# Optimization experiments

Hardware: AMD Instinct MI355X
Metric: run time of the kernel (lower is better)

## Reference

```python
import jax, jax.numpy as jnp
import numpy as np

N_EMBED = 1024
N_HEAD = 16
HEAD_DIM = N_EMBED // N_HEAD


def setup_inputs() -> dict:
    key = jax.random.key(0)
    ks = jax.random.split(key, 6)
    B, T, C = 4, 2048, N_EMBED
    scale = 1.0 / np.sqrt(C)
    x = jax.random.normal(ks[0], (B, T, C), dtype=jnp.float32)
    # torch nn.Linear weights are [out, in]; y = x @ W.T
    Wk = jax.random.normal(ks[1], (C, C), dtype=jnp.float32) * scale
    Wq = jax.random.normal(ks[2], (C, C), dtype=jnp.float32) * scale
    Wv = jax.random.normal(ks[3], (C, C), dtype=jnp.float32) * scale
    Wp = jax.random.normal(ks[4], (C, C), dtype=jnp.float32) * scale
    bp = jax.random.normal(ks[5], (C,), dtype=jnp.float32) * 0.01
    return {"x": x, "Wk": Wk, "Wq": Wq, "Wv": Wv, "Wp": Wp, "bp": bp}


def reference(x, Wk, Wq, Wv, Wp, bp):
    B, T, C = x.shape
    H, D = N_HEAD, HEAD_DIM
    # QKV projections (torch Linear: x @ W.T), split heads -> [B, H, T, D]
    k = (x @ Wk.T).reshape(B, T, H, D).transpose(0, 2, 1, 3)
    q = (x @ Wq.T).reshape(B, T, H, D).transpose(0, 2, 1, 3)
    v = (x @ Wv.T).reshape(B, T, H, D).transpose(0, 2, 1, 3)
    # scaled scores [B, H, T, T]
    att = jnp.einsum('bhtd,bhsd->bhts', q, k) * (1.0 / np.sqrt(D))
    causal = jnp.tril(jnp.ones((T, T), dtype=bool))
    att = jnp.where(causal[None, None, :, :], att, -jnp.inf)
    att = jax.nn.softmax(att, axis=-1)
    out = jnp.einsum('bhts,bhsd->bhtd', att, v)  # [B, H, T, D]
    out = out.transpose(0, 2, 1, 3).reshape(B, T, C)
    out = out @ Wp.T + bp
    return out
```

## Files before the change

### kernel.cpp

```cpp
#include <hip/hip_runtime.h>

typedef __bf16 bf16_t;
typedef bf16_t bf16x4 __attribute__((ext_vector_type(4)));
typedef bf16_t bf16x8 __attribute__((ext_vector_type(8)));
typedef float f32x4 __attribute__((ext_vector_type(4)));

#define B_ 4
#define T_ 2048
#define C_ 1024
#define H_ 16
#define D_ 64

#define GLDS(g, l)                                                          \
  __builtin_amdgcn_global_load_lds(                                         \
      (const __attribute__((address_space(1))) void*)(g),                   \
      (__attribute__((address_space(3))) void*)(l), 16, 0, 0)

static __device__ __forceinline__ f32x4 mfma16(bf16x8 a, bf16x8 b, f32x4 c) {
  return __builtin_amdgcn_mfma_f32_16x16x32_bf16(a, b, c, 0, 0, 0);
}

static __device__ __forceinline__ float exp2_hw(float x) {
  float r;
  asm("v_exp_f32 %0, %1" : "=v"(r) : "v"(x));
  return r;
}

__global__ void cvt_all(const float* __restrict__ x, const float* __restrict__ wq,
                        const float* __restrict__ wk, const float* __restrict__ wv,
                        const float* __restrict__ wp, bf16_t* __restrict__ xb,
                        bf16_t* __restrict__ wqb, bf16_t* __restrict__ wkb,
                        bf16_t* __restrict__ wvb, bf16_t* __restrict__ wpb) {
  int i = blockIdx.x * blockDim.x + threadIdx.x;
  const float* src;
  bf16_t* dst;
  int off;
  if (i < 2097152) {
    src = x; dst = xb; off = i;
  } else {
    int r = i - 2097152;
    int region = r >> 18;
    off = r & 262143;
    if (region == 0) { src = wq; dst = wqb; }
    else if (region == 1) { src = wk; dst = wkb; }
    else if (region == 2) { src = wv; dst = wvb; }
    else { src = wp; dst = wpb; }
  }
  float4 v = ((const float4*)src)[off];
  bf16x4 o = {(bf16_t)v.x, (bf16_t)v.y, (bf16_t)v.z, (bf16_t)v.w};
  ((bf16x4*)dst)[off] = o;
}

__global__ __launch_bounds__(512, 4) void gemm_qkv(
    const bf16_t* __restrict__ xb, const bf16_t* __restrict__ wq,
    const bf16_t* __restrict__ wk, const bf16_t* __restrict__ wv,
    bf16_t* __restrict__ qo, bf16_t* __restrict__ ko, bf16_t* __restrict__ vt) {
  __shared__ bf16_t lA[2][128 * 64];
  __shared__ bf16_t lB[2][3][64 * 64];
  const int tid = threadIdx.x, wave = tid >> 6, lane = tid & 63;
  const int g = lane >> 4;
  const int bid = blockIdx.x;
  const int swz = ((bid & 7) << 7) | (bid >> 3);
  const int col0 = (swz & 15) * 64, row0 = (swz >> 4) * 128;
  const int wr = wave >> 2, wc = wave & 3;
  f32x4 acc[3][4] = {};

  const int soffA[2] = {wave * 1024, (8 + wave) * 1024};
  size_t sgoA[2];
#pragma unroll
  for (int i = 0; i < 2; ++i) {
    const int lin = soffA[i] + lane * 16;
    const int r = lin >> 7;
    const int c = ((lin >> 4) & 7) ^ (r & 7);
    sgoA[i] = (size_t)r * C_ + c * 8;
  }
  const int soffB = wave * 1024;
  size_t sgoB;
  {
    const int lin = soffB + lane * 16;
    const int r = lin >> 7;
    const int c = ((lin >> 4) & 7) ^ (r & 7);
    sgoB = (size_t)r * C_ + c * 8;
  }
  int koffA[2][4], koffB[2];
#pragma unroll
  for (int s = 0; s < 2; ++s) {
    const int c = s * 4 + g;
#pragma unroll
    for (int m = 0; m < 4; ++m) {
      const int r = wr * 64 + m * 16 + (lane & 15);
      koffA[s][m] = r * 128 + ((c ^ (r & 7)) << 4);
    }
    const int rb = wc * 16 + (lane & 15);
    koffB[s] = rb * 128 + ((c ^ (rb & 7)) << 4);
  }

#define QKV_STAGE(k0, b)                                                    \
  {                                                                         \
    GLDS(xb + (size_t)row0 * C_ + (k0) + sgoA[0], &lA[b][soffA[0] >> 1]);   \
    GLDS(xb + (size_t)row0 * C_ + (k0) + sgoA[1], &lA[b][soffA[1] >> 1]);   \
    GLDS(wq + (size_t)col0 * C_ + (k0) + sgoB, &lB[b][0][soffB >> 1]);      \
    GLDS(wk + (size_t)col0 * C_ + (k0) + sgoB, &lB[b][1][soffB >> 1]);      \
    GLDS(wv + (size_t)col0 * C_ + (k0) + sgoB, &lB[b][2][soffB >> 1]);      \
  }

  QKV_STAGE(0, 0);
  int cur = 0;
  for (int k0 = 0; k0 < C_; k0 += 64) {
    __syncthreads();
    if (k0 + 64 < C_) QKV_STAGE(k0 + 64, cur ^ 1);
#pragma unroll
    for (int s = 0; s < 2; ++s) {
      const char* ab = (const char*)lA[cur];
      bf16x8 af[4];
#pragma unroll
      for (int m = 0; m < 4; ++m) af[m] = *(const bf16x8*)(ab + koffA[s][m]);
#pragma unroll
      for (int z = 0; z < 3; ++z) {
        bf16x8 bf = *(const bf16x8*)((const char*)lB[cur][z] + koffB[s]);
#pragma unroll
        for (int m = 0; m < 4; ++m) acc[z][m] = mfma16(af[m], bf, acc[z][m]);
      }
    }
    cur ^= 1;
  }
#pragma unroll
  for (int z = 0; z < 3; ++z) {
    bf16_t* outb = (z == 0) ? qo : ((z == 1) ? ko : vt);
    const float qs = (z == 0) ? 0.125f * 1.4426950408889634f : 1.0f;
    const int gc = col0 + wc * 16 + (lane & 15);
    const int h = gc >> 6, d = gc & 63;
#pragma unroll
    for (int m = 0; m < 4; ++m) {
      const int gr = row0 + wr * 64 + m * 16 + ((lane >> 4) << 2);
      const int b = gr >> 11, t = gr & (T_ - 1);
      if (z < 2) {
#pragma unroll
        for (int j = 0; j < 4; ++j)
          outb[(((size_t)(b * H_ + h)) * T_ + (t + j)) * D_ + d] =
              (bf16_t)(acc[z][m][j] * qs);
      } else {
        bf16x4 pk = {(bf16_t)acc[z][m][0], (bf16_t)acc[z][m][1],
                     (bf16_t)acc[z][m][2], (bf16_t)acc[z][m][3]};
        *(bf16x4*)(outb + (((size_t)(b * H_ + h)) * D_ + d) * T_ + t) = pk;
      }
    }
  }
}

__global__ __launch_bounds__(256) void gemm_proj(const bf16_t* __restrict__ att,
                                                 const bf16_t* __restrict__ wp,
                                                 const float* __restrict__ bias,
                                                 float* __restrict__ out) {
  __shared__ bf16_t lA[2][128 * 64];
  __shared__ bf16_t lB[2][128 * 64];
  const int tid = threadIdx.x;
  const int wave = tid >> 6, lane = tid & 63;
  const int wr = wave >> 1, wc = wave & 1;
  const int row0 = blockIdx.y * 128, col0 = blockIdx.x * 128;
  f32x4 acc[4][4] = {};

  const int soff[4] = {wave * 1024, (4 + wave) * 1024, (8 + wave) * 1024,
                       (12 + wave) * 1024};
  size_t sgo[4];
#pragma unroll
  for (int i = 0; i < 4; ++i) {
    const int lin = soff[i] + lane * 16;
    const int r = lin >> 7;
    const int c = ((lin >> 4) & 7) ^ (r & 7);
    sgo[i] = (size_t)r * C_ + c * 8;
  }

#define PROJ_STAGE(k0, b)                                                   \
  {                                                                         \
    _Pragma("unroll") for (int i = 0; i < 4; ++i) {                         \
      GLDS(att + (size_t)row0 * C_ + (k0) + sgo[i], &lA[b][soff[i] >> 1]);  \
      GLDS(wp + (size_t)col0 * C_ + (k0) + sgo[i], &lB[b][soff[i] >> 1]);   \
    }                                                                       \
  }

  PROJ_STAGE(0, 0);
  int cur = 0;
  for (int k0 = 0; k0 < C_; k0 += 64) {
    __syncthreads();
    if (k0 + 64 < C_) PROJ_STAGE(k0 + 64, cur ^ 1);
#pragma unroll
    for (int s = 0; s < 2; ++s) {
      bf16x8 af[4], bfr[4];
#pragma unroll
      for (int m = 0; m < 4; ++m) {
        const int r = wr * 64 + m * 16 + (lane & 15);
        const int c = s * 4 + (lane >> 4);
        af[m] = *(const bf16x8*)((const char*)lA[cur] + r * 128 +
                                 ((c ^ (r & 7)) << 4));
      }
#pragma unroll
      for (int n = 0; n < 4; ++n) {
        const int r = wc * 64 + n * 16 + (lane & 15);
        const int c = s * 4 + (lane >> 4);
        bfr[n] = *(const bf16x8*)((const char*)lB[cur] + r * 128 +
                                  ((c ^ (r & 7)) << 4));
      }
#pragma unroll
      for (int m = 0; m < 4; ++m)
#pragma unroll
        for (int n = 0; n < 4; ++n) acc[m][n] = mfma16(af[m], bfr[n], acc[m][n]);
    }
    cur ^= 1;
  }
#pragma unroll
  for (int m = 0; m < 4; ++m) {
#pragma unroll
    for (int n = 0; n < 4; ++n) {
      const int gr = row0 + wr * 64 + m * 16 + ((lane >> 4) << 2);
      const int gc = col0 + wc * 64 + n * 16 + (lane & 15);
      const float bv = bias[gc];
#pragma unroll
      for (int j = 0; j < 4; ++j)
        out[(size_t)(gr + j) * C_ + gc] = acc[m][n][j] + bv;
    }
  }
}

__global__ __launch_bounds__(512, 4) void attn_fwd(
    const bf16_t* __restrict__ Q, const bf16_t* __restrict__ K,
    const bf16_t* __restrict__ V, bf16_t* __restrict__ AO) {
  __shared__ bf16_t lK[2][2][64 * 64];
  __shared__ bf16_t lV[2][2][64 * 64];
  __shared__ bf16_t lP[8][16 * 64];
  const int tid = threadIdx.x, wave = tid >> 6, lane = tid & 63;
  const int g = lane >> 4;
  const int bh = blockIdx.y;
  const size_t baseK = (size_t)bh * T_ * D_;
  const size_t baseV = (size_t)bh * D_ * T_;
  const int bb = bh >> 4, hh = bh & 15;

  bf16x8 vones;
#pragma unroll
  for (int e = 0; e < 8; ++e) vones[e] = (bf16_t)1.0f;

  int koff[2][4];
#pragma unroll
  for (int s = 0; s < 2; ++s)
#pragma unroll
    for (int nf = 0; nf < 4; ++nf) {
      const int r = nf * 16 + (lane & 15);
      const int c = s * 4 + g;
      koff[s][nf] = r * 128 + ((c ^ (r & 7)) << 4);
    }
  int pwoff[4];
  {
    const int r = lane & 15;
#pragma unroll
    for (int nf = 0; nf < 4; ++nf)
      pwoff[nf] = r * 128 + (((2 * nf + (g >> 1)) ^ (r & 7)) << 4) +
                  ((g & 1) << 3);
  }
  const int soff = wave * 1024;
  const int slin = soff + lane * 16;
  const int srow = slin >> 7;
  const int scol = ((slin >> 4) & 7) ^ (srow & 7);
  const size_t kgo = (size_t)srow * D_ + scol * 8;
  const size_t vgo = (size_t)srow * T_ + scol * 8;

  for (int half = 0; half < 2; ++half) {
    const int qt = half ? (15 - blockIdx.x) : blockIdx.x;
    const int twv = qt * 128 + wave * 16;
    const int ntiles = qt + 1;
    __syncthreads();
#pragma unroll
    for (int sub = 0; sub < 2; ++sub) {
      GLDS(K + baseK + (size_t)sub * 64 * D_ + kgo, &lK[0][sub][soff >> 1]);
      GLDS(V + baseV + (size_t)sub * 64 + vgo, &lV[0][sub][soff >> 1]);
    }
    bf16x8 qf[2];
#pragma unroll
    for (int s = 0; s < 2; ++s)
      qf[s] = *(const bf16x8*)(Q + baseK +
                               (size_t)(twv + (lane & 15)) * D_ + s * 32 +
                               (g << 3));
    f32x4 lacc = {};
    f32x4 o[4] = {};
    int cur = 0;
    for (int it = 0; it < ntiles; ++it) {
      __syncthreads();
      if (it + 1 < ntiles) {
        const int nb = cur ^ 1;
        const size_t ks = (size_t)(it + 1) * 128;
#pragma unroll
        for (int sub = 0; sub < 2; ++sub) {
          GLDS(K + baseK + (ks + sub * 64) * D_ + kgo,
               &lK[nb][sub][soff >> 1]);
          GLDS(V + baseV + ks + sub * 64 + vgo, &lV[nb][sub][soff >> 1]);
        }
      }
      const int s0 = it * 128;
      f32x4 sc[2][4];
#pragma unroll
      for (int sub = 0; sub < 2; ++sub)
#pragma unroll
        for (int nf = 0; nf < 4; ++nf) sc[sub][nf] = (f32x4){};
      __builtin_amdgcn_s_setprio(1);
#pragma unroll
      for (int sub = 0; sub < 2; ++sub) {
        const char* kb = (const char*)lK[cur][sub];
#pragma unroll
        for (int s = 0; s < 2; ++s)
#pragma unroll
          for (int nf = 0; nf < 4; ++nf)
            sc[sub][nf] =
                mfma16(*(const bf16x8*)(kb + koff[s][nf]), qf[s], sc[sub][nf]);
      }
      __builtin_amdgcn_s_setprio(0);
      if (it == qt) {
        const int t = twv + (lane & 15);
#pragma unroll
        for (int sub = 0; sub < 2; ++sub)
#pragma unroll
          for (int nf = 0; nf < 4; ++nf)
#pragma unroll
            for (int j = 0; j < 4; ++j) {
              const int s = s0 + sub * 64 + nf * 16 + g * 4 + j;
              if (s > t) sc[sub][nf][j] = -1e30f;
            }
      }
      bf16x4 pk[2][4];
#pragma unroll
      for (int sub = 0; sub < 2; ++sub)
#pragma unroll
        for (int nf = 0; nf < 4; ++nf) {
          pk[sub][nf][0] = (bf16_t)exp2_hw(sc[sub][nf][0]);
          pk[sub][nf][1] = (bf16_t)exp2_hw(sc[sub][nf][1]);
          pk[sub][nf][2] = (bf16_t)exp2_hw(sc[sub][nf][2]);
          pk[sub][nf][3] = (bf16_t)exp2_hw(sc[sub][nf][3]);
        }
      __builtin_amdgcn_s_setprio(1);
#pragma unroll
      for (int sub = 0; sub < 2; ++sub) {
        char* pw = (char*)lP[wave];
#pragma unroll
        for (int nf = 0; nf < 4; ++nf) *(bf16x4*)(pw + pwoff[nf]) = pk[sub][nf];
        const char* pb = (const char*)lP[wave];
        const char* vb = (const char*)lV[cur][sub];
#pragma unroll
        for (int s2 = 0; s2 < 2; ++s2) {
          bf16x8 pf = *(const bf16x8*)(pb + koff[s2][0]);
          lacc = mfma16(pf, vones, lacc);
#pragma unroll
          for (int df = 0; df < 4; ++df)
            o[df] = mfma16(pf, *(const bf16x8*)(vb + koff[s2][df]), o[df]);
        }
      }
      __builtin_amdgcn_s_setprio(0);
      cur ^= 1;
    }
    {
#pragma unroll
      for (int j = 0; j < 4; ++j) {
        const float inv = 1.0f / lacc[j];
        const int t = twv + (g << 2) + j;
#pragma unroll
        for (int df = 0; df < 4; ++df) {
          const int cc = hh * 64 + df * 16 + (lane & 15);
          AO[((size_t)(bb * T_ + t)) * C_ + cc] = (bf16_t)(o[df][j] * inv);
        }
      }
    }
  }
}

extern "C" void kernel_launch(void* const* d_in, const int* in_sizes, int n_in,
                              void* d_out, int out_size, void* d_ws,
                              size_t ws_size, hipStream_t stream) {
  const float* x = (const float*)d_in[0];
  const float* Wk = (const float*)d_in[1];
  const float* Wq = (const float*)d_in[2];
  const float* Wv = (const float*)d_in[3];
  const float* Wp = (const float*)d_in[4];
  const float* bp = (const float*)d_in[5];
  char* ws = (char*)d_ws;
  bf16_t* xb = (bf16_t*)ws;
  bf16_t* wqb = (bf16_t*)(ws + (16u << 20));
  bf16_t* wkb = (bf16_t*)(ws + (18u << 20));
  bf16_t* wvb = (bf16_t*)(ws + (20u << 20));
  bf16_t* wpb = (bf16_t*)(ws + (22u << 20));
  bf16_t* q = (bf16_t*)(ws + (24u << 20));
  bf16_t* k = (bf16_t*)(ws + (40u << 20));
  bf16_t* vt = (bf16_t*)(ws + (56u << 20));
  bf16_t* att = xb;

  cvt_all<<<12288, 256, 0, stream>>>(x, Wq, Wk, Wv, Wp, xb, wqb, wkb, wvb, wpb);
  gemm_qkv<<<1024, 512, 0, stream>>>(xb, wqb, wkb, wvb, q, k, vt);
  attn_fwd<<<dim3(8, 64), 512, 0, stream>>>(q, k, vt, att);
  gemm_proj<<<dim3(8, 64), 256, 0, stream>>>(att, wpb, bp, (float*)d_out);
}
```

Baseline: 159.3 us.

## Shrink attention KV tile to 64 keys and raise occupancy hint

Changes the attention kernel's per-iteration key/value tile from 128 keys (two 64-key sub-tiles) to a single 64-key tile, doubling the iteration count and halving the double-buffered LDS footprint. It also raises the launch-bounds occupancy hint from 4 to 6 blocks so more waves can fit per CU. The aim is to lower register and LDS pressure for better latency hiding. In exchange it adds more barriers and loop overhead per key processed, and the causal mask now covers the last two tiles.

Measured after the change: 162.7 us. 2.1% more time.

```diff
diff --git a/kernel.cpp b/kernel.cpp
--- a/kernel.cpp
+++ b/kernel.cpp
@@ -222,11 +222,11 @@
   }
 }
 
-__global__ __launch_bounds__(512, 4) void attn_fwd(
+__global__ __launch_bounds__(512, 6) void attn_fwd(
     const bf16_t* __restrict__ Q, const bf16_t* __restrict__ K,
     const bf16_t* __restrict__ V, bf16_t* __restrict__ AO) {
-  __shared__ bf16_t lK[2][2][64 * 64];
-  __shared__ bf16_t lV[2][2][64 * 64];
+  __shared__ bf16_t lK[2][64 * 64];
+  __shared__ bf16_t lV[2][64 * 64];
   __shared__ bf16_t lP[8][16 * 64];
   const int tid = threadIdx.x, wave = tid >> 6, lane = tid & 63;
   const int g = lane >> 4;
@@ -266,13 +266,10 @@
   for (int half = 0; half < 2; ++half) {
     const int qt = half ? (15 - blockIdx.x) : blockIdx.x;
     const int twv = qt * 128 + wave * 16;
-    const int ntiles = qt + 1;
+    const int ntiles = 2 * qt + 2;
     __syncthreads();
-#pragma unroll
-    for (int sub = 0; sub < 2; ++sub) {
-      GLDS(K + baseK + (size_t)sub * 64 * D_ + kgo, &lK[0][sub][soff >> 1]);
-      GLDS(V + baseV + (size_t)sub * 64 + vgo, &lV[0][sub][soff >> 1]);
-    }
+    GLDS(K + baseK + kgo, &lK[0][soff >> 1]);
+    GLDS(V + baseV + vgo, &lV[0][soff >> 1]);
     bf16x8 qf[2];
 #pragma unroll
     for (int s = 0; s < 2; ++s)
@@ -286,70 +283,55 @@
       __syncthreads();
       if (it + 1 < ntiles) {
         const int nb = cur ^ 1;
-        const size_t ks = (size_t)(it + 1) * 128;
-#pragma unroll
-        for (int sub = 0; sub < 2; ++sub) {
-          GLDS(K + baseK + (ks + sub * 64) * D_ + kgo,
-               &lK[nb][sub][soff >> 1]);
-          GLDS(V + baseV + ks + sub * 64 + vgo, &lV[nb][sub][soff >> 1]);
-        }
-      }
-      const int s0 = it * 128;
-      f32x4 sc[2][4];
-#pragma unroll
-      for (int sub = 0; sub < 2; ++sub)
-#pragma unroll
-        for (int nf = 0; nf < 4; ++nf) sc[sub][nf] = (f32x4){};
+        GLDS(K + baseK + (size_t)(it + 1) * 64 * D_ + kgo,
+             &lK[nb][soff >> 1]);
+        GLDS(V + baseV + (size_t)(it + 1) * 64 + vgo, &lV[nb][soff >> 1]);
+      }
+      const char* kb = (const char*)lK[cur];
+      const char* vb = (const char*)lV[cur];
+      const int s0 = it * 64;
+      f32x4 sc[4];
+#pragma unroll
+      for (int nf = 0; nf < 4; ++nf) sc[nf] = (f32x4){};
       __builtin_amdgcn_s_setprio(1);
 #pragma unroll
-      for (int sub = 0; sub < 2; ++sub) {
-        const char* kb = (const char*)lK[cur][sub];
-#pragma unroll
-        for (int s = 0; s < 2; ++s)
-#pragma unroll
-          for (int nf = 0; nf < 4; ++nf)
-            sc[sub][nf] =
-                mfma16(*(const bf16x8*)(kb + koff[s][nf]), qf[s], sc[sub][nf]);
-      }
+      for (int s = 0; s < 2; ++s)
+#pragma unroll
+        for (int nf = 0; nf < 4; ++nf)
+          sc[nf] = mfma16(*(const bf16x8*)(kb + koff[s][nf]), qf[s], sc[nf]);
       __builtin_amdgcn_s_setprio(0);
-      if (it == qt) {
+      if (it >= 2 * qt) {
         const int t = twv + (lane & 15);
 #pragma unroll
-        for (int sub = 0; sub < 2; ++sub)
-#pragma unroll
-          for (int nf = 0; nf < 4; ++nf)
-#pragma unroll
-            for (int j = 0; j < 4; ++j) {
-              const int s = s0 + sub * 64 + nf * 16 + g * 4 + j;
-              if (s > t) sc[sub][nf][j] = -1e30f;
-            }
-      }
-      bf16x4 pk[2][4];
-#pragma unroll
-      for (int sub = 0; sub < 2; ++sub)
-#pragma unroll
-        for (int nf = 0; nf < 4; ++nf) {
-          pk[sub][nf][0] = (bf16_t)exp2_hw(sc[sub][nf][0]);
-          pk[sub][nf][1] = (bf16_t)exp2_hw(sc[sub][nf][1]);
-          pk[sub][nf][2] = (bf16_t)exp2_hw(sc[sub][nf][2]);
-          pk[sub][nf][3] = (bf16_t)exp2_hw(sc[sub][nf][3]);
-        }
+        for (int nf = 0; nf < 4; ++nf)
+#pragma unroll
+          for (int j = 0; j < 4; ++j) {
+            const int s = s0 + nf * 16 + g * 4 + j;
+            if (s > t) sc[nf][j] = -1e30f;
+          }
+      }
+      bf16x4 pk[4];
+#pragma unroll
+      for (int nf = 0; nf < 4; ++nf) {
+        pk[nf][0] = (bf16_t)exp2_hw(sc[nf][0]);
+        pk[nf][1] = (bf16_t)exp2_hw(sc[nf][1]);
+        pk[nf][2] = (bf16_t)exp2_hw(sc[nf][2]);
+        pk[nf][3] = (bf16_t)exp2_hw(sc[nf][3]);
+      }
+      {
+        char* pw = (char*)lP[wave];
+#pragma unroll
+        for (int nf = 0; nf < 4; ++nf) *(bf16x4*)(pw + pwoff[nf]) = pk[nf];
+      }
       __builtin_amdgcn_s_setprio(1);
-#pragma unroll
-      for (int sub = 0; sub < 2; ++sub) {
-        char* pw = (char*)lP[wave];
-#pragma unroll
-        for (int nf = 0; nf < 4; ++nf) *(bf16x4*)(pw + pwoff[nf]) = pk[sub][nf];
-        const char* pb = (const char*)lP[wave];
-        const char* vb = (const char*)lV[cur][sub];
-#pragma unroll
-        for (int s2 = 0; s2 < 2; ++s2) {
-          bf16x8 pf = *(const bf16x8*)(pb + koff[s2][0]);
-          lacc = mfma16(pf, vones, lacc);
-#pragma unroll
-          for (int df = 0; df < 4; ++df)
-            o[df] = mfma16(pf, *(const bf16x8*)(vb + koff[s2][df]), o[df]);
-        }
+      const char* pb = (const char*)lP[wave];
+#pragma unroll
+      for (int s2 = 0; s2 < 2; ++s2) {
+        bf16x8 pf = *(const bf16x8*)(pb + koff[s2][0]);
+        lacc = mfma16(pf, vones, lacc);
+#pragma unroll
+        for (int df = 0; df < 4; ++df)
+          o[df] = mfma16(pf, *(const bf16x8*)(vb + koff[s2][df]), o[df]);
       }
       __builtin_amdgcn_s_setprio(0);
       cur ^= 1;
```
